# Optimization experiments

Measured on AMD Instinct MI355X. Metric: run time of the kernel, lower is better.

The kernel has to match this reference:

```python
import jax, jax.numpy as jnp
import numpy as np

B, S, H = 8, 2048, 768

def setup_inputs() -> dict:
    key = jax.random.key(0)
    ks = jax.random.split(key, 11)
    queries = jax.random.normal(ks[0], (B, S, H), dtype=jnp.float32)
    keys_ = jax.random.normal(ks[1], (B, S, H), dtype=jnp.float32)
    values = jax.random.normal(ks[2], (B, S, H), dtype=jnp.float32)
    coordinates = jax.random.uniform(ks[3], (B, S, 2), dtype=jnp.float32)
    scale = 1.0 / np.sqrt(H)
    Wq = jax.random.normal(ks[4], (H, H), dtype=jnp.float32) * scale
    bq = jnp.zeros((H,), dtype=jnp.float32)
    Wk = jax.random.normal(ks[5], (H, H), dtype=jnp.float32) * scale
    bk = jnp.zeros((H,), dtype=jnp.float32)
    Wv = jax.random.normal(ks[6], (H, H), dtype=jnp.float32) * scale
    bv = jnp.zeros((H,), dtype=jnp.float32)
    spatial_weight = jax.random.normal(ks[7], (1,), dtype=jnp.float32)
    return {"queries": queries, "keys": keys_, "values": values,
            "coordinates": coordinates, "Wq": Wq, "bq": bq, "Wk": Wk,
            "bk": bk, "Wv": Wv, "bv": bv, "spatial_weight": spatial_weight}

def _cdist(c):
    # c: [B, S, 2] -> pairwise euclidean distances [B, S, S]
    sq = jnp.sum(c * c, axis=-1)  # [B, S]
    d2 = sq[:, :, None] + sq[:, None, :] - 2.0 * jnp.einsum('bsd,btd->bst', c, c)
    return jnp.sqrt(jnp.maximum(d2, 1e-12))

def reference(queries, keys, values, coordinates, Wq, bq, Wk, bk, Wv, bv, spatial_weight):
    q = queries @ Wq.T + bq  # [B, S, H]
    k = keys @ Wk.T + bk
    v = values @ Wv.T + bv
    scores = jnp.einsum('bsh,bth->bst', q, k)          # [B, S, S]
    scores = scores - spatial_weight[0] * _cdist(coordinates)
    attn = jax.nn.softmax(scores, axis=-1)
    out = jnp.einsum('bst,bth->bsh', attn, v)          # [B, S, H]
    return out, attn
```

## Files before the change

kernel.cpp:

```cpp
#include <hip/hip_runtime.h>
#include <stdint.h>


typedef _Float16 half8 __attribute__((ext_vector_type(8)));
typedef _Float16 half4v __attribute__((ext_vector_type(4)));
typedef float f32x4 __attribute__((ext_vector_type(4)));

#define DEVI static __device__ __forceinline__

constexpr int B_ = 8, S_ = 2048, H_ = 768;
constexpr long NX = (long)B_ * S_ * H_;
constexpr long NW = (long)H_ * H_;
constexpr long ATT = (long)B_ * S_ * S_;

DEVI void glds16(const void* g, void* l) {
  __builtin_amdgcn_global_load_lds(
      (const __attribute__((address_space(1))) uint32_t*)g,
      (__attribute__((address_space(3))) uint32_t*)l, 16, 0, 0);
}

DEVI void stage_tile(const _Float16* gbase, int rowStride, _Float16* lds, int tid) {
#pragma unroll
  for (int seg = 0; seg < 2; ++seg) {
    int u = seg * 256 + tid;
    int r = u >> 2, c = u & 3;
    int sc = c ^ ((r >> 1) & 3);
    glds16(gbase + (long)r * rowStride + sc * 8, lds + ((u & ~63) << 3));
  }
}

DEVI half8 frag(const _Float16* lds, int m0, int lane) {
  int row = m0 + (lane & 15);
  int c = (lane >> 4) ^ ((row >> 1) & 3);
  return *(const half8*)(lds + row * 32 + c * 8);
}

__global__ __launch_bounds__(256) void k_split(
    const float* __restrict__ xq, const float* __restrict__ xk,
    const float* __restrict__ xv, const float* __restrict__ wq,
    const float* __restrict__ wk, const float* __restrict__ wv,
    _Float16* __restrict__ dst) {
  const long NX4 = NX / 4, NW4 = NW / 4, TOT = 3 * NX4 + 3 * NW4;
  for (long u = (long)blockIdx.x * blockDim.x + threadIdx.x; u < TOT;
       u += (long)gridDim.x * blockDim.x) {
    const float4* src;
    _Float16 *dh, *dl;
    bool wantLo = true;
    long idx;
    if (u < 3 * NX4) {
      int z = (u >= 2 * NX4) ? 2 : (u >= NX4) ? 1 : 0;
      idx = u - (long)z * NX4;
      src = (const float4*)(z == 0 ? xq : z == 1 ? xk : xv);
      dh = dst + (long)z * 2 * NX;
      dl = dh + NX;
      wantLo = (z < 2);
    } else {
      long t = u - 3 * NX4;
      int z = (t >= 2 * NW4) ? 2 : (t >= NW4) ? 1 : 0;
      idx = t - (long)z * NW4;
      src = (const float4*)(z == 0 ? wq : z == 1 ? wk : wv);
      dh = dst + 5 * NX + (long)z * 2 * NW;
      dl = dh + NW;
      wantLo = (z < 2);
    }
    float4 x = src[idx];
    half4v hi, lo;
    hi[0] = (_Float16)x.x; lo[0] = (_Float16)(x.x - (float)hi[0]);
    hi[1] = (_Float16)x.y; lo[1] = (_Float16)(x.y - (float)hi[1]);
    hi[2] = (_Float16)x.z; lo[2] = (_Float16)(x.z - (float)hi[2]);
    hi[3] = (_Float16)x.w; lo[3] = (_Float16)(x.w - (float)hi[3]);
    *(half4v*)(dh + idx * 4) = hi;
    if (wantLo) *(half4v*)(dl + idx * 4) = lo;
  }
}

__global__ __launch_bounds__(256, 2) void k_proj(
    const _Float16* __restrict__ scratch, const float* __restrict__ bq,
    const float* __restrict__ bk, const float* __restrict__ bv,
    _Float16* __restrict__ qh, _Float16* __restrict__ ql,
    _Float16* __restrict__ kh, _Float16* __restrict__ kl,
    _Float16* __restrict__ vT) {
  const int nt = blockIdx.x, mt = blockIdx.y, z = blockIdx.z;
  const int tid = threadIdx.x;
  const bool full = (z < 2);
  const _Float16* Xh = scratch + (long)z * 2 * NX;
  const _Float16* Xl = Xh + NX;
  const _Float16* Wh = scratch + 5 * NX + (long)z * 2 * NW;
  const _Float16* Wl = Wh + NW;
  const float* bias = (z == 0) ? bq : (z == 1) ? bk : bv;

  __shared__ _Float16 sm[2][4][4096];
  f32x4 acc[4][4] = {};

  const _Float16* Ah = Xh + (long)(mt * 128) * H_;
  const _Float16* Al = Xl + (long)(mt * 128) * H_;
  const _Float16* Bh = Wh + (long)(nt * 128) * H_;
  const _Float16* Bl = Wl + (long)(nt * 128) * H_;

  stage_tile(Ah, H_, sm[0][0], tid);
  stage_tile(Bh, H_, sm[0][2], tid);
  if (full) {
    stage_tile(Al, H_, sm[0][1], tid);
    stage_tile(Bl, H_, sm[0][3], tid);
  }
  __syncthreads();

  const int lane = tid & 63, wid = tid >> 6;
  const int wm = (wid >> 1) * 64, wn = (wid & 1) * 64;

  int cur = 0;
  for (int kk = 0; kk < 24; ++kk) {
    if (kk + 1 < 24) {
      int o = (kk + 1) * 32;
      stage_tile(Ah + o, H_, sm[cur ^ 1][0], tid);
      stage_tile(Bh + o, H_, sm[cur ^ 1][2], tid);
      if (full) {
        stage_tile(Al + o, H_, sm[cur ^ 1][1], tid);
        stage_tile(Bl + o, H_, sm[cur ^ 1][3], tid);
      }
    }
    half8 ah[4], bh[4];
#pragma unroll
    for (int i = 0; i < 4; ++i) ah[i] = frag(sm[cur][0], wm + i * 16, lane);
#pragma unroll
    for (int j = 0; j < 4; ++j) bh[j] = frag(sm[cur][2], wn + j * 16, lane);
#pragma unroll
    for (int i = 0; i < 4; ++i)
#pragma unroll
      for (int j = 0; j < 4; ++j)
        acc[i][j] = __builtin_amdgcn_mfma_f32_16x16x32_f16(ah[i], bh[j],
                                                           acc[i][j], 0, 0, 0);
    if (full) {
      half8 al[4], bl[4];
#pragma unroll
      for (int i = 0; i < 4; ++i) al[i] = frag(sm[cur][1], wm + i * 16, lane);
#pragma unroll
      for (int j = 0; j < 4; ++j) bl[j] = frag(sm[cur][3], wn + j * 16, lane);
#pragma unroll
      for (int i = 0; i < 4; ++i)
#pragma unroll
        for (int j = 0; j < 4; ++j) {
          acc[i][j] = __builtin_amdgcn_mfma_f32_16x16x32_f16(ah[i], bl[j],
                                                             acc[i][j], 0, 0, 0);
          acc[i][j] = __builtin_amdgcn_mfma_f32_16x16x32_f16(al[i], bh[j],
                                                             acc[i][j], 0, 0, 0);
        }
    }
    __syncthreads();
    cur ^= 1;
  }

  _Float16* oh = (z == 0) ? qh : kh;
  _Float16* ol = (z == 0) ? ql : kl;
#pragma unroll
  for (int i = 0; i < 4; ++i) {
    int m_t = wm + i * 16 + ((lane >> 4) << 2);
#pragma unroll
    for (int j = 0; j < 4; ++j) {
      int n_t = wn + j * 16 + (lane & 15);
      int gn = nt * 128 + n_t;
      float bs = bias[gn];
      if (full) {
#pragma unroll
        for (int r = 0; r < 4; ++r) {
          long gm = (long)mt * 128 + m_t + r;
          float y = acc[i][j][r] + bs;
          _Float16 hi = (_Float16)y;
          oh[gm * H_ + gn] = hi;
          ol[gm * H_ + gn] = (_Float16)(y - (float)hi);
        }
      } else {
        int gmI = mt * 128 + m_t;
        int bb = gmI >> 11, t0 = gmI & 2047;
        half4v pk;
#pragma unroll
        for (int r = 0; r < 4; ++r) pk[r] = (_Float16)(acc[i][j][r] + bs);
        *(half4v*)&vT[((long)bb * H_ + gn) * S_ + t0] = pk;
      }
    }
  }
}

__global__ __launch_bounds__(512, 2) void k_scores8p(
    const _Float16* __restrict__ qh, const _Float16* __restrict__ ql,
    const _Float16* __restrict__ kh_, const _Float16* __restrict__ kl_,
    const float* __restrict__ coords, const float* __restrict__ sw,
    float* __restrict__ attn) {
  const int nt = blockIdx.x, mt = blockIdx.y, b = blockIdx.z;
  const int tid = threadIdx.x, lane = tid & 63, wid = tid >> 6;
  const int wr = wid >> 2, wc = wid & 3;

  __shared__ _Float16 lds[2][2][2][8192];
  __shared__ float cco[4][256];

  if (tid < 256) {
    long gi = (long)b * S_ + mt * 256 + tid;
    cco[0][tid] = coords[gi * 2 + 0];
    cco[1][tid] = coords[gi * 2 + 1];
  } else {
    int t = tid - 256;
    long gj = (long)b * S_ + nt * 256 + t;
    cco[2][t] = coords[gj * 2 + 0];
    cco[3][t] = coords[gj * 2 + 1];
  }
  const float w = sw[0];

  const long aoff = ((long)b * S_ + mt * 256) * H_;
  const long boff = ((long)b * S_ + nt * 256) * H_;

  long goff[2];
  int loff[2];
#pragma unroll
  for (int seg = 0; seg < 2; ++seg) {
    int u = seg * 512 + tid;
    int r = u >> 2, c = u & 3;
    int sc = c ^ ((r >> 1) & 3);
    goff[seg] = (long)r * H_ + sc * 8;
    loff[seg] = (u & ~63) << 3;
  }

  f32x4 acc[8][4] = {};

  auto stage_half = [&](int h) {
    int th = h >> 2, kind = h & 3;
    int khf = kind >> 1, mx = kind & 1;
    int term = th % 3;
    long ko = (long)(th / 3) * 64 + khf * 32;
    const _Float16* src = mx ? ((term == 1 ? kl_ : kh_) + boff + ko)
                             : ((term == 2 ? ql : qh) + aoff + ko);
    _Float16* dst = &lds[th & 1][khf][mx][0];
    glds16(src + goff[0], dst + loff[0]);
    glds16(src + goff[1], dst + loff[1]);
  };

  half8 bf[4];

  auto phase = [&](int slot, int kh, int mh, int hst, int vm) {
    const _Float16* A = &lds[slot][kh][0][0];
    const _Float16* Bt = &lds[slot][kh][1][0];
    half8 af[4];
    if (mh == 0) {
#pragma unroll
      for (int j = 0; j < 4; ++j) bf[j] = frag(Bt, wc * 64 + j * 16, lane);
    }
#pragma unroll
    for (int i = 0; i < 4; ++i)
      af[i] = frag(A, wr * 128 + mh * 64 + i * 16, lane);
    if (hst >= 0) stage_half(hst);
    if (vm == 6) asm volatile("s_waitcnt vmcnt(6)" ::: "memory");
    else if (vm == 0) asm volatile("s_waitcnt vmcnt(0)" ::: "memory");
    __builtin_amdgcn_s_barrier();
    asm volatile("s_waitcnt lgkmcnt(0)" ::: "memory");
    __builtin_amdgcn_sched_barrier(0);
    __builtin_amdgcn_s_setprio(1);
#pragma unroll
    for (int i = 0; i < 4; ++i)
#pragma unroll
      for (int j = 0; j < 4; ++j)
        acc[mh * 4 + i][j] = __builtin_amdgcn_mfma_f32_16x16x32_f16(
            af[i], bf[j], acc[mh * 4 + i][j], 0, 0, 0);
    __builtin_amdgcn_s_setprio(0);
    asm volatile("" ::: "memory");
    __builtin_amdgcn_s_barrier();
  };

#pragma unroll
  for (int h = 0; h < 7; ++h) stage_half(h);
  asm volatile("s_waitcnt vmcnt(6)" ::: "memory");
  __builtin_amdgcn_s_barrier();

#pragma unroll 1
  for (int t = 0; t < 34; ++t) {
    const int slot = t & 1, P = 4 * t;
    phase(slot, 0, 0, P + 7, -1);
    phase(slot, 0, 1, P + 8, -1);
    phase(slot, 1, 0, P + 9, -1);
    phase(slot, 1, 1, P + 10 <= 143 ? P + 10 : -1, 6);
  }
  phase(0, 0, 0, 143, -1);
  phase(0, 0, 1, -1, -1);
  phase(0, 1, 0, -1, -1);
  phase(0, 1, 1, -1, 0);
  phase(1, 0, 0, -1, -1);
  phase(1, 0, 1, -1, -1);
  phase(1, 1, 0, -1, -1);
  phase(1, 1, 1, -1, -1);

#pragma unroll
  for (int mi = 0; mi < 8; ++mi) {
    int m_t = wr * 128 + mi * 16 + ((lane >> 4) << 2);
#pragma unroll
    for (int j = 0; j < 4; ++j) {
      int n_t = wc * 64 + j * 16 + (lane & 15);
      float cjx = cco[2][n_t], cjy = cco[3][n_t];
      long rowbase = ((long)b * S_ + mt * 256 + m_t) * S_ + nt * 256 + n_t;
#pragma unroll
      for (int r = 0; r < 4; ++r) {
        float dx = cco[0][m_t + r] - cjx;
        float dy = cco[1][m_t + r] - cjy;
        float d = sqrtf(fmaxf(fmaf(dx, dx, dy * dy), 1e-12f));
        attn[rowbase + (long)r * S_] = acc[mi][j][r] - w * d;
      }
    }
  }
}

__global__ __launch_bounds__(256) void k_rowsoft(float* __restrict__ attn,
                                                 _Float16* __restrict__ a16) {
  const int wid = threadIdx.x >> 6, lane = threadIdx.x & 63;
  long row = (long)blockIdx.x * 4 + wid;
  float* p = attn + row * S_;
  _Float16* p16 = a16 + row * S_;
  float4 v[8];
#pragma unroll
  for (int i = 0; i < 8; ++i) v[i] = ((const float4*)p)[i * 64 + lane];
  float m = -3.4e38f;
#pragma unroll
  for (int i = 0; i < 8; ++i)
    m = fmaxf(m, fmaxf(fmaxf(v[i].x, v[i].y), fmaxf(v[i].z, v[i].w)));
#pragma unroll
  for (int o = 32; o > 0; o >>= 1) m = fmaxf(m, __shfl_xor(m, o));
  float l = 0.f;
#pragma unroll
  for (int i = 0; i < 8; ++i) {
    v[i].x = __expf(v[i].x - m);
    v[i].y = __expf(v[i].y - m);
    v[i].z = __expf(v[i].z - m);
    v[i].w = __expf(v[i].w - m);
    l += (v[i].x + v[i].y) + (v[i].z + v[i].w);
  }
#pragma unroll
  for (int o = 32; o > 0; o >>= 1) l += __shfl_xor(l, o);
  const float rl = 1.0f / l;
#pragma unroll
  for (int i = 0; i < 8; ++i) {
    v[i].x *= rl; v[i].y *= rl; v[i].z *= rl; v[i].w *= rl;
    ((float4*)p)[i * 64 + lane] = v[i];
    half4v h = {(_Float16)v[i].x, (_Float16)v[i].y, (_Float16)v[i].z,
                (_Float16)v[i].w};
    ((half4v*)p16)[i * 64 + lane] = h;
  }
}

__global__ __launch_bounds__(256, 2) void k_pv16(
    const _Float16* __restrict__ a16, const _Float16* __restrict__ vT,
    float* __restrict__ outp) {
  const int nt = blockIdx.x, mt = blockIdx.y, b = blockIdx.z;
  const int tid = threadIdx.x, lane = tid & 63, wid = tid >> 6;
  const int wm = (wid >> 1) * 64, wn = (wid & 1) * 64;
  __shared__ _Float16 sm[2][2][4096];
  f32x4 acc[4][4] = {};
  const _Float16* Ab = a16 + ((long)b * S_ + mt * 128) * S_;
  const _Float16* Bb = vT + ((long)b * H_ + nt * 128) * S_;

  stage_tile(Ab, S_, sm[0][0], tid);
  stage_tile(Bb, S_, sm[0][1], tid);
  __syncthreads();

  int cur = 0;
  for (int kk = 0; kk < 64; ++kk) {
    if (kk + 1 < 64) {
      stage_tile(Ab + (kk + 1) * 32, S_, sm[cur ^ 1][0], tid);
      stage_tile(Bb + (kk + 1) * 32, S_, sm[cur ^ 1][1], tid);
    }
    half8 ah[4], bh[4];
#pragma unroll
    for (int i = 0; i < 4; ++i) ah[i] = frag(sm[cur][0], wm + i * 16, lane);
#pragma unroll
    for (int j = 0; j < 4; ++j) bh[j] = frag(sm[cur][1], wn + j * 16, lane);
#pragma unroll
    for (int i = 0; i < 4; ++i)
#pragma unroll
      for (int j = 0; j < 4; ++j)
        acc[i][j] = __builtin_amdgcn_mfma_f32_16x16x32_f16(ah[i], bh[j],
                                                           acc[i][j], 0, 0, 0);
    __syncthreads();
    cur ^= 1;
  }

#pragma unroll
  for (int i = 0; i < 4; ++i) {
    int m_t = wm + i * 16 + ((lane >> 4) << 2);
#pragma unroll
    for (int j = 0; j < 4; ++j) {
      int n_t = wn + j * 16 + (lane & 15);
      int h = nt * 128 + n_t;
      long rowbase = (long)b * S_ + mt * 128 + m_t;
#pragma unroll
      for (int r = 0; r < 4; ++r) outp[(rowbase + r) * H_ + h] = acc[i][j][r];
    }
  }
}

extern "C" void kernel_launch(void* const* d_in, const int* in_sizes, int n_in,
                              void* d_out, int out_size, void* d_ws,
                              size_t ws_size, hipStream_t stream) {
  const float* xq = (const float*)d_in[0];
  const float* xk = (const float*)d_in[1];
  const float* xv = (const float*)d_in[2];
  const float* co = (const float*)d_in[3];
  const float* wq = (const float*)d_in[4];
  const float* bq = (const float*)d_in[5];
  const float* wk = (const float*)d_in[6];
  const float* bk = (const float*)d_in[7];
  const float* wv = (const float*)d_in[8];
  const float* bv = (const float*)d_in[9];
  const float* sw = (const float*)d_in[10];

  float* out = (float*)d_out;
  float* attn = out + NX;
  _Float16* scratch = (_Float16*)d_out;

  _Float16* qh = (_Float16*)d_ws;
  _Float16* ql = qh + NX;
  _Float16* kh = ql + NX;
  _Float16* kl = kh + NX;
  _Float16* vT = kl + NX;
  _Float16* a16 = qh;

  k_split<<<dim3(2048), 256, 0, stream>>>(xq, xk, xv, wq, wk, wv, scratch);
  k_proj<<<dim3(6, 128, 3), 256, 0, stream>>>(scratch, bq, bk, bv, qh, ql, kh,
                                              kl, vT);
  k_scores8p<<<dim3(8, 8, 8), 512, 0, stream>>>(qh, ql, kh, kl, co, sw, attn);
  k_rowsoft<<<dim3(4096), 256, 0, stream>>>(attn, a16);
  k_pv16<<<dim3(6, 16, 8), 256, 0, stream>>>(a16, vT, out);
}
```

Measured before the change: 505.0 us.

## Port projection GEMM to 256x256 eight-phase pipelined schedule and swizzle block order

Replaces the 128x128 double-buffered projection kernel with a 512-thread 256x256-tile variant that reuses the phased global_load_lds pipeline from the scores kernel. The split-precision terms (hi*hi, hi*lo, lo*hi) become separate streamed K-steps instead of being computed together per tile. It also remaps block IDs in the scores and PV kernels so consecutive blocks land on different XCDs, aiming for better L2 locality. The larger tile raises register pressure, and the projection grid drops to 576 blocks.

```diff
diff --git a/kernel.cpp b/kernel.cpp
--- a/kernel.cpp
+++ b/kernel.cpp
@@ -74,107 +74,133 @@
   }
 }
 
-__global__ __launch_bounds__(256, 2) void k_proj(
+__global__ __launch_bounds__(512, 2) void k_proj8p(
     const _Float16* __restrict__ scratch, const float* __restrict__ bq,
     const float* __restrict__ bk, const float* __restrict__ bv,
     _Float16* __restrict__ qh, _Float16* __restrict__ ql,
     _Float16* __restrict__ kh, _Float16* __restrict__ kl,
     _Float16* __restrict__ vT) {
-  const int nt = blockIdx.x, mt = blockIdx.y, z = blockIdx.z;
-  const int tid = threadIdx.x;
+  const int ntw = blockIdx.x, z = blockIdx.y, mt = blockIdx.z;
+  const int tid = threadIdx.x, lane = tid & 63, wid = tid >> 6;
+  const int wr = wid >> 2, wc = wid & 3;
   const bool full = (z < 2);
-  const _Float16* Xh = scratch + (long)z * 2 * NX;
-  const _Float16* Xl = Xh + NX;
-  const _Float16* Wh = scratch + 5 * NX + (long)z * 2 * NW;
-  const _Float16* Wl = Wh + NW;
+  const int NT = full ? 36 : 12;
+
+  const _Float16* Ah = scratch + (long)z * 2 * NX;
+  const _Float16* Al = Ah + NX;
+  const _Float16* Bh = scratch + 5 * NX + (long)z * 2 * NW;
+  const _Float16* Bl = Bh + NW;
   const float* bias = (z == 0) ? bq : (z == 1) ? bk : bv;
 
-  __shared__ _Float16 sm[2][4][4096];
-  f32x4 acc[4][4] = {};
-
-  const _Float16* Ah = Xh + (long)(mt * 128) * H_;
-  const _Float16* Al = Xl + (long)(mt * 128) * H_;
-  const _Float16* Bh = Wh + (long)(nt * 128) * H_;
-  const _Float16* Bl = Wl + (long)(nt * 128) * H_;
-
-  stage_tile(Ah, H_, sm[0][0], tid);
-  stage_tile(Bh, H_, sm[0][2], tid);
-  if (full) {
-    stage_tile(Al, H_, sm[0][1], tid);
-    stage_tile(Bl, H_, sm[0][3], tid);
-  }
-  __syncthreads();
-
-  const int lane = tid & 63, wid = tid >> 6;
-  const int wm = (wid >> 1) * 64, wn = (wid & 1) * 64;
-
-  int cur = 0;
-  for (int kk = 0; kk < 24; ++kk) {
-    if (kk + 1 < 24) {
-      int o = (kk + 1) * 32;
-      stage_tile(Ah + o, H_, sm[cur ^ 1][0], tid);
-      stage_tile(Bh + o, H_, sm[cur ^ 1][2], tid);
-      if (full) {
-        stage_tile(Al + o, H_, sm[cur ^ 1][1], tid);
-        stage_tile(Bl + o, H_, sm[cur ^ 1][3], tid);
-      }
-    }
-    half8 ah[4], bh[4];
-#pragma unroll
-    for (int i = 0; i < 4; ++i) ah[i] = frag(sm[cur][0], wm + i * 16, lane);
-#pragma unroll
-    for (int j = 0; j < 4; ++j) bh[j] = frag(sm[cur][2], wn + j * 16, lane);
+  __shared__ _Float16 lds[2][2][2][8192];
+
+  const long aoff = (long)(mt * 256) * H_;
+  const long boff = (long)(ntw * 256) * H_;
+
+  long goff[2];
+  int loff[2];
+#pragma unroll
+  for (int seg = 0; seg < 2; ++seg) {
+    int u = seg * 512 + tid;
+    int r = u >> 2, c = u & 3;
+    int sc = c ^ ((r >> 1) & 3);
+    goff[seg] = (long)r * H_ + sc * 8;
+    loff[seg] = (u & ~63) << 3;
+  }
+
+  f32x4 acc[8][4] = {};
+
+  auto stage_half = [&](int h) {
+    int th = h >> 2, kind = h & 3;
+    int khf = kind >> 1, mx = kind & 1;
+    int term, ko;
+    if (full) { term = th % 3; ko = (th / 3) * 64 + khf * 32; }
+    else { term = 0; ko = th * 64 + khf * 32; }
+    const _Float16* src = mx ? ((term == 1 ? Bl : Bh) + boff + ko)
+                             : ((term == 2 ? Al : Ah) + aoff + ko);
+    _Float16* dst = &lds[th & 1][khf][mx][0];
+    glds16(src + goff[0], dst + loff[0]);
+    glds16(src + goff[1], dst + loff[1]);
+  };
+
+  half8 bf[4];
+
+  auto phase = [&](int slot, int kh2, int mh, int hst, int vm) {
+    const _Float16* A = &lds[slot][kh2][0][0];
+    const _Float16* Bt = &lds[slot][kh2][1][0];
+    half8 af[4];
+    if (mh == 0) {
+#pragma unroll
+      for (int j = 0; j < 4; ++j) bf[j] = frag(Bt, wc * 64 + j * 16, lane);
+    }
 #pragma unroll
     for (int i = 0; i < 4; ++i)
+      af[i] = frag(A, wr * 128 + mh * 64 + i * 16, lane);
+    if (hst >= 0) stage_half(hst);
+    if (vm == 6) asm volatile("s_waitcnt vmcnt(6)" ::: "memory");
+    else if (vm == 0) asm volatile("s_waitcnt vmcnt(0)" ::: "memory");
+    __builtin_amdgcn_s_barrier();
+    asm volatile("s_waitcnt lgkmcnt(0)" ::: "memory");
+    __builtin_amdgcn_sched_barrier(0);
+    __builtin_amdgcn_s_setprio(1);
+#pragma unroll
+    for (int i = 0; i < 4; ++i)
 #pragma unroll
       for (int j = 0; j < 4; ++j)
-        acc[i][j] = __builtin_amdgcn_mfma_f32_16x16x32_f16(ah[i], bh[j],
-                                                           acc[i][j], 0, 0, 0);
-    if (full) {
-      half8 al[4], bl[4];
-#pragma unroll
-      for (int i = 0; i < 4; ++i) al[i] = frag(sm[cur][1], wm + i * 16, lane);
-#pragma unroll
-      for (int j = 0; j < 4; ++j) bl[j] = frag(sm[cur][3], wn + j * 16, lane);
-#pragma unroll
-      for (int i = 0; i < 4; ++i)
-#pragma unroll
-        for (int j = 0; j < 4; ++j) {
-          acc[i][j] = __builtin_amdgcn_mfma_f32_16x16x32_f16(ah[i], bl[j],
-                                                             acc[i][j], 0, 0, 0);
-          acc[i][j] = __builtin_amdgcn_mfma_f32_16x16x32_f16(al[i], bh[j],
-                                                             acc[i][j], 0, 0, 0);
-        }
-    }
-    __syncthreads();
-    cur ^= 1;
-  }
+        acc[mh * 4 + i][j] = __builtin_amdgcn_mfma_f32_16x16x32_f16(
+            af[i], bf[j], acc[mh * 4 + i][j], 0, 0, 0);
+    __builtin_amdgcn_s_setprio(0);
+    asm volatile("" ::: "memory");
+    __builtin_amdgcn_s_barrier();
+  };
+
+#pragma unroll
+  for (int h = 0; h < 7; ++h) stage_half(h);
+  asm volatile("s_waitcnt vmcnt(6)" ::: "memory");
+  __builtin_amdgcn_s_barrier();
+
+#pragma unroll 1
+  for (int t = 0; t < NT - 2; ++t) {
+    const int slot = t & 1, P = 4 * t;
+    phase(slot, 0, 0, P + 7, -1);
+    phase(slot, 0, 1, P + 8, -1);
+    phase(slot, 1, 0, P + 9, -1);
+    phase(slot, 1, 1, P + 10, 6);
+  }
+  phase(0, 0, 0, 4 * NT - 1, -1);
+  phase(0, 0, 1, -1, -1);
+  phase(0, 1, 0, -1, -1);
+  phase(0, 1, 1, -1, 0);
+  phase(1, 0, 0, -1, -1);
+  phase(1, 0, 1, -1, -1);
+  phase(1, 1, 0, -1, -1);
+  phase(1, 1, 1, -1, -1);
 
   _Float16* oh = (z == 0) ? qh : kh;
   _Float16* ol = (z == 0) ? ql : kl;
 #pragma unroll
-  for (int i = 0; i < 4; ++i) {
-    int m_t = wm + i * 16 + ((lane >> 4) << 2);
+  for (int mi = 0; mi < 8; ++mi) {
+    int m_t = wr * 128 + mi * 16 + ((lane >> 4) << 2);
 #pragma unroll
     for (int j = 0; j < 4; ++j) {
-      int n_t = wn + j * 16 + (lane & 15);
-      int gn = nt * 128 + n_t;
+      int n_t = wc * 64 + j * 16 + (lane & 15);
+      int gn = ntw * 256 + n_t;
       float bs = bias[gn];
       if (full) {
 #pragma unroll
         for (int r = 0; r < 4; ++r) {
-          long gm = (long)mt * 128 + m_t + r;
-          float y = acc[i][j][r] + bs;
+          long gm = (long)mt * 256 + m_t + r;
+          float y = acc[mi][j][r] + bs;
           _Float16 hi = (_Float16)y;
           oh[gm * H_ + gn] = hi;
           ol[gm * H_ + gn] = (_Float16)(y - (float)hi);
         }
       } else {
-        int gmI = mt * 128 + m_t;
+        int gmI = mt * 256 + m_t;
         int bb = gmI >> 11, t0 = gmI & 2047;
         half4v pk;
 #pragma unroll
-        for (int r = 0; r < 4; ++r) pk[r] = (_Float16)(acc[i][j][r] + bs);
+        for (int r = 0; r < 4; ++r) pk[r] = (_Float16)(acc[mi][j][r] + bs);
         *(half4v*)&vT[((long)bb * H_ + gn) * S_ + t0] = pk;
       }
     }
@@ -186,7 +212,9 @@
     const _Float16* __restrict__ kh_, const _Float16* __restrict__ kl_,
     const float* __restrict__ coords, const float* __restrict__ sw,
     float* __restrict__ attn) {
-  const int nt = blockIdx.x, mt = blockIdx.y, b = blockIdx.z;
+  int bid = blockIdx.x + 8 * blockIdx.y + 64 * blockIdx.z;
+  int swz = (bid & 7) * 64 + (bid >> 3);
+  const int nt = swz & 7, mt = (swz >> 3) & 7, b = swz >> 6;
   const int tid = threadIdx.x, lane = tid & 63, wid = tid >> 6;
   const int wr = wid >> 2, wc = wid & 3;
 
@@ -235,9 +263,9 @@
 
   half8 bf[4];
 
-  auto phase = [&](int slot, int kh, int mh, int hst, int vm) {
-    const _Float16* A = &lds[slot][kh][0][0];
-    const _Float16* Bt = &lds[slot][kh][1][0];
+  auto phase = [&](int slot, int kh2, int mh, int hst, int vm) {
+    const _Float16* A = &lds[slot][kh2][0][0];
+    const _Float16* Bt = &lds[slot][kh2][1][0];
     half8 af[4];
     if (mh == 0) {
 #pragma unroll
@@ -275,7 +303,7 @@
     phase(slot, 0, 0, P + 7, -1);
     phase(slot, 0, 1, P + 8, -1);
     phase(slot, 1, 0, P + 9, -1);
-    phase(slot, 1, 1, P + 10 <= 143 ? P + 10 : -1, 6);
+    phase(slot, 1, 1, P + 10, 6);
   }
   phase(0, 0, 0, 143, -1);
   phase(0, 0, 1, -1, -1);
@@ -345,7 +373,9 @@
 __global__ __launch_bounds__(256, 2) void k_pv16(
     const _Float16* __restrict__ a16, const _Float16* __restrict__ vT,
     float* __restrict__ outp) {
-  const int nt = blockIdx.x, mt = blockIdx.y, b = blockIdx.z;
+  int bid = blockIdx.x + 6 * blockIdx.y + 96 * blockIdx.z;
+  int swz = (bid & 7) * 96 + (bid >> 3);
+  const int nt = swz % 6, mt = (swz / 6) & 15, b = swz / 96;
   const int tid = threadIdx.x, lane = tid & 63, wid = tid >> 6;
   const int wm = (wid >> 1) * 64, wn = (wid & 1) * 64;
   __shared__ _Float16 sm[2][2][4096];
@@ -419,8 +449,8 @@
   _Float16* a16 = qh;
 
   k_split<<<dim3(2048), 256, 0, stream>>>(xq, xk, xv, wq, wk, wv, scratch);
-  k_proj<<<dim3(6, 128, 3), 256, 0, stream>>>(scratch, bq, bk, bv, qh, ql, kh,
-                                              kl, vT);
+  k_proj8p<<<dim3(3, 3, 64), 512, 0, stream>>>(scratch, bq, bk, bv, qh, ql, kh,
+                                               kl, vT);
   k_scores8p<<<dim3(8, 8, 8), 512, 0, stream>>>(qh, ql, kh, kl, co, sw, attn);
   k_rowsoft<<<dim3(4096), 256, 0, stream>>>(attn, a16);
   k_pv16<<<dim3(6, 16, 8), 256, 0, stream>>>(a16, vT, out);
```

Result: slower. 741.6 us (+46.8%).
